# Performance work log

Hardware: AMD Instinct MI355X
Metric: run time of the kernel (lower is better)

Reference implementation:

```python
import math
import jax, jax.numpy as jnp
import numpy as np

CAPACITY_FACTOR = 1.0
MIN_CAPACITY = 4


def setup_inputs() -> dict:
    key = jax.random.key(0)
    k1, k2 = jax.random.split(key)
    x = jax.random.normal(k1, (8192, 1024), dtype=jnp.float32)
    wg = jax.random.normal(k2, (1024, 64), dtype=jnp.float32) * 0.02
    return {"x": x, "wg": wg}


def reference(x, wg):
    # Gate projection: [S, D] @ [D, E] -> [S, E]
    logits = x @ wg
    S, E = logits.shape
    # _capacity: ceil(S / E * capacity_factor * 2) for top-2, floored at min_capacity (static)
    capacity = max(math.ceil((S / E) * (CAPACITY_FACTOR * 2.0)), MIN_CAPACITY)

    gates = jax.nn.softmax(logits, axis=-1)           # [S, E]
    org_gates = gates

    # top-1 expert
    indices1_s = jnp.argmax(gates, axis=1)
    mask1 = jax.nn.one_hot(indices1_s, E, dtype=jnp.int32)
    # top-2 expert (deterministic: no gumbel sampling)
    logits_except1 = jnp.where(mask1.astype(bool), -jnp.inf, logits)
    indices2_s = jnp.argmax(logits_except1, axis=1)
    mask2 = jax.nn.one_hot(indices2_s, E, dtype=jnp.int32)

    # per-expert running positions
    locations1 = jnp.cumsum(mask1, axis=0) - 1        # [S, E]
    locations2 = jnp.cumsum(mask2, axis=0) - 1 + jnp.sum(mask1, axis=0, keepdims=True)

    # load-balancing aux loss
    me = jnp.mean(gates, axis=0)
    ce = jnp.mean(mask1.astype(gates.dtype), axis=0)
    l_aux = jnp.sum(me * ce) * E * E

    exp_counts = jnp.sum(mask1 + mask2, axis=0)

    # drop tokens over capacity
    mask1 = mask1 * (locations1 < capacity).astype(jnp.int32)
    mask2 = mask2 * (locations2 < capacity).astype(jnp.int32)

    locations1_s = jnp.sum(locations1 * mask1, axis=1)  # [S]
    locations2_s = jnp.sum(locations2 * mask2, axis=1)

    mask1_f = mask1.astype(gates.dtype)
    mask2_f = mask2.astype(gates.dtype)
    gates1_s = jnp.sum(gates * mask1_f, axis=1)
    gates2_s = jnp.sum(gates * mask2_f, axis=1)
    denom_s = jnp.clip(gates1_s + gates2_s, jnp.finfo(gates.dtype).eps)
    gates1_s = gates1_s / denom_s
    gates2_s = gates2_s / denom_s

    gates1 = gates1_s[:, None] * mask1_f              # [S, E]
    gates2 = gates2_s[:, None] * mask2_f

    locations1_sc = jax.nn.one_hot(locations1_s, capacity, dtype=gates.dtype)  # [S, C]
    locations2_sc = jax.nn.one_hot(locations2_s, capacity, dtype=gates.dtype)

    combine_weights = (jnp.einsum('se,sc->sec', gates1, locations1_sc)
                       + jnp.einsum('se,sc->sec', gates2, locations2_sc))  # [S, E, C]
    dispatch_mask = combine_weights.astype(bool)
    return l_aux, combine_weights, dispatch_mask, exp_counts, org_gates
```

## Files before the change

kernel.cpp:

```cpp
#include <hip/hip_runtime.h>
#include <math.h>

#define S_TOKENS 8192
#define D_DIM    1024
#define E_EXP    64
#define CAPACITY 256
#define TPB      64
#define NBLK     (S_TOKENS / TPB)
#define NZBLK    4096

typedef float fx4 __attribute__((ext_vector_type(4)));

#define SZ_COMBINE   (134217728LL)
#define OFF_COMBINE  (1LL)
#define OFF_DISPATCH (OFF_COMBINE + SZ_COMBINE)
#define OFF_EXPCNT   (OFF_DISPATCH + SZ_COMBINE)
#define OFF_ORGGATES (OFF_EXPCNT + E_EXP)

#define WS_IDX1 0
#define WS_IDX2 (WS_IDX1 + S_TOKENS)
#define WS_G1   (WS_IDX2 + S_TOKENS)
#define WS_G2   (WS_G1 + S_TOKENS)
#define WS_CNT1 (WS_G2 + S_TOKENS)
#define WS_CNT2 (WS_CNT1 + NBLK * E_EXP)
#define WS_OFF1 (WS_CNT2 + NBLK * E_EXP)
#define WS_OFF2 (WS_OFF1 + NBLK * E_EXP)
#define WS_MEP  (WS_OFF2 + NBLK * E_EXP)

__global__ __launch_bounds__(256) void k1_gemm_gate(
    const float* __restrict__ x, const float* __restrict__ wg,
    float* __restrict__ out, int* __restrict__ wsi, float* __restrict__ wsf) {
  const int bid = blockIdx.x;
  const int tid = threadIdx.x;

  if (bid >= NBLK) {
    fx4 z = (fx4)0.f;
    fx4* p = (fx4*)out;
    const size_t n4 = (size_t)(2 * SZ_COMBINE) / 4;
    const size_t nth = (size_t)NZBLK * 256;
    for (size_t i = (size_t)(bid - NBLK) * 256 + tid; i < n4; i += nth)
      __builtin_nontemporal_store(z, &p[i]);
    if (bid == NBLK && tid == 0) out[2 * SZ_COMBINE] = 0.0f;
    return;
  }

  __shared__ float xs[64][68];
  __shared__ float ovl[64 * 68];
  __shared__ float mM[64], rS[64];
  __shared__ int   li1[64], li2[64];
  __shared__ float mered[16][64];

  float (*wsh)[64] = (float(*)[64])ovl;
  float (*Lg)[68]  = (float(*)[68])ovl;

  const int tx = tid & 15;
  const int ty = tid >> 4;
  const int s0 = bid * TPB;

  float acc[4][4];
#pragma unroll
  for (int i = 0; i < 4; i++)
#pragma unroll
    for (int q = 0; q < 4; q++) acc[i][q] = 0.f;

  for (int k0 = 0; k0 < D_DIM; k0 += 64) {
#pragma unroll
    for (int r = 0; r < 4; r++) {
      int i = tid + 256 * r;
      int t = i >> 4, c = i & 15;
      *(fx4*)&xs[t][4 * c] =
          *(const fx4*)&x[(size_t)(s0 + t) * D_DIM + k0 + 4 * c];
      *(fx4*)&wsh[t][4 * c] =
          *(const fx4*)&wg[(size_t)(k0 + t) * E_EXP + 4 * c];
    }
    __syncthreads();
    for (int kb = 0; kb < 64; kb += 4) {
      fx4 xa[4], wb[4];
#pragma unroll
      for (int i = 0; i < 4; i++) xa[i] = *(fx4*)&xs[ty + 16 * i][kb];
#pragma unroll
      for (int j = 0; j < 4; j++) wb[j] = *(fx4*)&wsh[kb + j][4 * tx];
#pragma unroll
      for (int j = 0; j < 4; j++)
#pragma unroll
        for (int i = 0; i < 4; i++) {
          float xv = xa[i][j];
#pragma unroll
          for (int q = 0; q < 4; q++)
            acc[i][q] = fmaf(xv, wb[j][q], acc[i][q]);
        }
    }
    __syncthreads();
  }

#pragma unroll
  for (int i = 0; i < 4; i++) {
    fx4 v;
#pragma unroll
    for (int q = 0; q < 4; q++) v[q] = acc[i][q];
    *(fx4*)&Lg[ty + 16 * i][4 * tx] = v;
  }
  __syncthreads();

  {
    const int g = tid >> 2;
    const int u = tid & 3;
    float bv = -INFINITY; int bi = 0;
#pragma unroll
    for (int i = 0; i < 16; i++) {
      int ee = u + 4 * i;
      float v = Lg[g][ee];
      if (v > bv) { bv = v; bi = ee; }
    }
#pragma unroll
    for (int d = 1; d < 4; d <<= 1) {
      float ovv = __shfl_xor(bv, d, 4);
      int   oi  = __shfl_xor(bi, d, 4);
      if (ovv > bv || (ovv == bv && oi < bi)) { bv = ovv; bi = oi; }
    }
    const float m1 = bv; const int i1 = bi;

    float se = 0.f;
#pragma unroll
    for (int i = 0; i < 16; i++) se += expf(Lg[g][u + 4 * i] - m1);
#pragma unroll
    for (int d = 1; d < 4; d <<= 1) se += __shfl_xor(se, d, 4);

    float bv2 = -INFINITY; int bi2 = 0;
#pragma unroll
    for (int i = 0; i < 16; i++) {
      int ee = u + 4 * i;
      float v = Lg[g][ee];
      if (ee != i1 && v > bv2) { bv2 = v; bi2 = ee; }
    }
#pragma unroll
    for (int d = 1; d < 4; d <<= 1) {
      float ovv = __shfl_xor(bv2, d, 4);
      int   oi  = __shfl_xor(bi2, d, 4);
      if (ovv > bv2 || (ovv == bv2 && oi < bi2)) { bv2 = ovv; bi2 = oi; }
    }

    if (u == 0) {
      float rs = 1.0f / se;
      mM[g] = m1; rS[g] = rs;
      li1[g] = i1; li2[g] = bi2;
      int s = s0 + g;
      wsi[WS_IDX1 + s] = i1;
      wsi[WS_IDX2 + s] = bi2;
      wsf[WS_G1 + s] = rs;
      wsf[WS_G2 + s] = expf(bv2 - m1) * rs;
    }
  }
  __syncthreads();

  {
    float ms[4] = {0.f, 0.f, 0.f, 0.f};
#pragma unroll
    for (int i = 0; i < 4; i++) {
      int t = ty + 16 * i;
      float m = mM[t], r = rS[t];
      size_t ob = OFF_ORGGATES + (size_t)(s0 + t) * E_EXP + 4 * tx;
#pragma unroll
      for (int q = 0; q < 4; q++) {
        float gate = expf(Lg[t][4 * tx + q] - m) * r;
        out[ob + q] = gate;
        ms[q] += gate;
      }
    }
#pragma unroll
    for (int q = 0; q < 4; q++) mered[ty][4 * tx + q] = ms[q];
  }
  __syncthreads();

  if (tid < 64) {
    float s = 0.f;
#pragma unroll
    for (int yy = 0; yy < 16; yy++) s += mered[yy][tid];
    wsf[WS_MEP + bid * 64 + tid] = s;
    int c1 = 0, c2 = 0;
    for (int t = 0; t < TPB; t++) {
      c1 += (li1[t] == tid);
      c2 += (li2[t] == tid);
    }
    wsi[WS_CNT1 + bid * 64 + tid] = c1;
    wsi[WS_CNT2 + bid * 64 + tid] = c2;
  }
}

__global__ __launch_bounds__(1024) void k2_scan(
    float* __restrict__ out, int* __restrict__ wsi, float* __restrict__ wsf) {
  __shared__ int lc[NBLK * E_EXP];
  __shared__ float mep[16][E_EXP];
  __shared__ int tot1[E_EXP];

  const int tid = threadIdx.x;

  {
    const int e = tid & 63, cg = tid >> 6;
    float s = 0.f;
#pragma unroll
    for (int c = cg * 8; c < cg * 8 + 8; c++) s += wsf[WS_MEP + c * 64 + e];
    mep[cg][e] = s;
  }

  {
    const int4* g = (const int4*)&wsi[WS_CNT1];
    int4* l = (int4*)lc;
#pragma unroll
    for (int i = tid; i < NBLK * E_EXP / 4; i += 1024) l[i] = g[i];
  }
  __syncthreads();

  if (tid < E_EXP) {
    int run = 0;
#pragma unroll 8
    for (int c = 0; c < NBLK; c++) {
      wsi[WS_OFF1 + c * 64 + tid] = run;
      run += lc[c * 64 + tid];
    }
    tot1[tid] = run;
  }
  __syncthreads();

  {
    const int4* g = (const int4*)&wsi[WS_CNT2];
    int4* l = (int4*)lc;
#pragma unroll
    for (int i = tid; i < NBLK * E_EXP / 4; i += 1024) l[i] = g[i];
  }
  __syncthreads();

  if (tid < E_EXP) {
    const int e = tid;
    const int total1 = tot1[e];
    int run = total1;
#pragma unroll 8
    for (int c = 0; c < NBLK; c++) {
      wsi[WS_OFF2 + c * 64 + e] = run;
      run += lc[c * 64 + e];
    }
    const int total2 = run - total1;

    out[OFF_EXPCNT + e] = (float)(total1 + total2);

    float mesum = 0.f;
#pragma unroll
    for (int cg = 0; cg < 16; cg++) mesum += mep[cg][e];
    float me = mesum * (1.0f / 8192.0f);
    float ce = (float)total1 * (1.0f / 8192.0f);
    float prod = me * ce * 4096.0f;
#pragma unroll
    for (int d = 1; d < 64; d <<= 1) prod += __shfl_xor(prod, d, 64);
    if (e == 0) out[0] = prod;
  }
}

__global__ __launch_bounds__(64) void k3_scatter(
    float* __restrict__ out, const int* __restrict__ wsi,
    const float* __restrict__ wsf) {
  __shared__ int li1[TPB], li2[TPB];
  const int bid = blockIdx.x;
  const int t = threadIdx.x;
  const int s0 = bid * TPB;

  li1[t] = wsi[WS_IDX1 + s0 + t];
  li2[t] = wsi[WS_IDX2 + s0 + t];
  __syncthreads();

  const int e1 = li1[t], e2 = li2[t];
  int r1 = 0, r2 = 0;
  for (int j = 0; j < t; j++) {
    r1 += (li1[j] == e1);
    r2 += (li2[j] == e2);
  }
  const int loc1 = wsi[WS_OFF1 + bid * 64 + e1] + r1;
  const int loc2 = wsi[WS_OFF2 + bid * 64 + e2] + r2;
  const int s = s0 + t;

  const float g1r = wsf[WS_G1 + s];
  const float g2r = wsf[WS_G2 + s];
  const bool d1 = (loc1 >= CAPACITY);
  const bool d2 = (loc2 >= CAPACITY);
  const float g1f = d1 ? 0.f : g1r;
  const float g2f = d2 ? 0.f : g2r;
  const float denom = fmaxf(g1f + g2f, 1.1920929e-7f);
  const float w1 = g1f / denom;
  const float w2 = g2f / denom;

  if (!d1) {
    size_t o = OFF_COMBINE + (size_t)s * (E_EXP * CAPACITY) +
               (size_t)e1 * CAPACITY + loc1;
    out[o] = w1;
    out[o + SZ_COMBINE] = (w1 != 0.f) ? 1.f : 0.f;
  }
  if (!d2) {
    size_t o = OFF_COMBINE + (size_t)s * (E_EXP * CAPACITY) +
               (size_t)e2 * CAPACITY + loc2;
    out[o] = w2;
    out[o + SZ_COMBINE] = (w2 != 0.f) ? 1.f : 0.f;
  }
}

extern "C" void kernel_launch(void* const* d_in, const int* in_sizes, int n_in,
                              void* d_out, int out_size, void* d_ws,
                              size_t ws_size, hipStream_t stream) {
  const float* x  = (const float*)d_in[0];
  const float* wg = (const float*)d_in[1];
  float* out = (float*)d_out;
  int*   wsi = (int*)d_ws;
  float* wsf = (float*)d_ws;

  hipLaunchKernelGGL(k1_gemm_gate, dim3(NBLK + NZBLK), dim3(256), 0, stream,
                     x, wg, out, wsi, wsf);
  hipLaunchKernelGGL(k2_scan, dim3(1), dim3(1024), 0, stream, out, wsi, wsf);
  hipLaunchKernelGGL(k3_scatter, dim3(NBLK), dim3(64), 0, stream, out, wsi,
                     wsf);
}
```

Measured before the change: 1.134 ms.

## Fuse scan and scatter kernels into one single-block kernel with LDS offsets

```diff
diff --git a/kernel.cpp b/kernel.cpp
--- a/kernel.cpp
+++ b/kernel.cpp
@@ -23,9 +23,7 @@
 #define WS_G2   (WS_G1 + S_TOKENS)
 #define WS_CNT1 (WS_G2 + S_TOKENS)
 #define WS_CNT2 (WS_CNT1 + NBLK * E_EXP)
-#define WS_OFF1 (WS_CNT2 + NBLK * E_EXP)
-#define WS_OFF2 (WS_OFF1 + NBLK * E_EXP)
-#define WS_MEP  (WS_OFF2 + NBLK * E_EXP)
+#define WS_MEP  (WS_CNT2 + NBLK * E_EXP)
 
 __global__ __launch_bounds__(256) void k1_gemm_gate(
     const float* __restrict__ x, const float* __restrict__ wg,
@@ -187,11 +185,12 @@
   }
 }
 
-__global__ __launch_bounds__(1024) void k2_scan(
-    float* __restrict__ out, int* __restrict__ wsi, float* __restrict__ wsf) {
-  __shared__ int lc[NBLK * E_EXP];
+__global__ __launch_bounds__(1024) void k23_scan_scatter(
+    float* __restrict__ out, const int* __restrict__ wsi,
+    const float* __restrict__ wsf) {
+  __shared__ int off1[NBLK * E_EXP];
+  __shared__ int off2[NBLK * E_EXP];
   __shared__ float mep[16][E_EXP];
-  __shared__ int tot1[E_EXP];
 
   const int tid = threadIdx.x;
 
@@ -204,42 +203,36 @@
   }
 
   {
-    const int4* g = (const int4*)&wsi[WS_CNT1];
-    int4* l = (int4*)lc;
-#pragma unroll
-    for (int i = tid; i < NBLK * E_EXP / 4; i += 1024) l[i] = g[i];
+    const int4* g1 = (const int4*)&wsi[WS_CNT1];
+    const int4* g2 = (const int4*)&wsi[WS_CNT2];
+    int4* l1 = (int4*)off1;
+    int4* l2 = (int4*)off2;
+#pragma unroll
+    for (int i = tid; i < NBLK * E_EXP / 4; i += 1024) {
+      l1[i] = g1[i];
+      l2[i] = g2[i];
+    }
   }
   __syncthreads();
 
   if (tid < E_EXP) {
+    const int e = tid;
     int run = 0;
 #pragma unroll 8
     for (int c = 0; c < NBLK; c++) {
-      wsi[WS_OFF1 + c * 64 + tid] = run;
-      run += lc[c * 64 + tid];
-    }
-    tot1[tid] = run;
-  }
-  __syncthreads();
-
-  {
-    const int4* g = (const int4*)&wsi[WS_CNT2];
-    int4* l = (int4*)lc;
-#pragma unroll
-    for (int i = tid; i < NBLK * E_EXP / 4; i += 1024) l[i] = g[i];
-  }
-  __syncthreads();
-
-  if (tid < E_EXP) {
-    const int e = tid;
-    const int total1 = tot1[e];
-    int run = total1;
+      int v = off1[c * 64 + e];
+      off1[c * 64 + e] = run;
+      run += v;
+    }
+    const int total1 = run;
+    int run2 = total1;
 #pragma unroll 8
     for (int c = 0; c < NBLK; c++) {
-      wsi[WS_OFF2 + c * 64 + e] = run;
-      run += lc[c * 64 + e];
-    }
-    const int total2 = run - total1;
+      int v = off2[c * 64 + e];
+      off2[c * 64 + e] = run2;
+      run2 += v;
+    }
+    const int total2 = run2 - total1;
 
     out[OFF_EXPCNT + e] = (float)(total1 + total2);
 
@@ -253,51 +246,46 @@
     for (int d = 1; d < 64; d <<= 1) prod += __shfl_xor(prod, d, 64);
     if (e == 0) out[0] = prod;
   }
-}
-
-__global__ __launch_bounds__(64) void k3_scatter(
-    float* __restrict__ out, const int* __restrict__ wsi,
-    const float* __restrict__ wsf) {
-  __shared__ int li1[TPB], li2[TPB];
-  const int bid = blockIdx.x;
-  const int t = threadIdx.x;
-  const int s0 = bid * TPB;
-
-  li1[t] = wsi[WS_IDX1 + s0 + t];
-  li2[t] = wsi[WS_IDX2 + s0 + t];
-  __syncthreads();
-
-  const int e1 = li1[t], e2 = li2[t];
-  int r1 = 0, r2 = 0;
-  for (int j = 0; j < t; j++) {
-    r1 += (li1[j] == e1);
-    r2 += (li2[j] == e2);
-  }
-  const int loc1 = wsi[WS_OFF1 + bid * 64 + e1] + r1;
-  const int loc2 = wsi[WS_OFF2 + bid * 64 + e2] + r2;
-  const int s = s0 + t;
-
-  const float g1r = wsf[WS_G1 + s];
-  const float g2r = wsf[WS_G2 + s];
-  const bool d1 = (loc1 >= CAPACITY);
-  const bool d2 = (loc2 >= CAPACITY);
-  const float g1f = d1 ? 0.f : g1r;
-  const float g2f = d2 ? 0.f : g2r;
-  const float denom = fmaxf(g1f + g2f, 1.1920929e-7f);
-  const float w1 = g1f / denom;
-  const float w2 = g2f / denom;
-
-  if (!d1) {
-    size_t o = OFF_COMBINE + (size_t)s * (E_EXP * CAPACITY) +
-               (size_t)e1 * CAPACITY + loc1;
-    out[o] = w1;
-    out[o + SZ_COMBINE] = (w1 != 0.f) ? 1.f : 0.f;
-  }
-  if (!d2) {
-    size_t o = OFF_COMBINE + (size_t)s * (E_EXP * CAPACITY) +
-               (size_t)e2 * CAPACITY + loc2;
-    out[o] = w2;
-    out[o + SZ_COMBINE] = (w2 != 0.f) ? 1.f : 0.f;
+  __syncthreads();
+
+  const int wv = tid >> 6, ln = tid & 63;
+  for (int c = wv; c < NBLK; c += 16) {
+    const int s = c * TPB + ln;
+    const int e1 = wsi[WS_IDX1 + s];
+    const int e2 = wsi[WS_IDX2 + s];
+    int r1 = 0, r2 = 0;
+#pragma unroll 7
+    for (int j = 0; j < TPB - 1; j++) {
+      int o1 = __shfl(e1, j, 64);
+      int o2 = __shfl(e2, j, 64);
+      r1 += (j < ln && o1 == e1);
+      r2 += (j < ln && o2 == e2);
+    }
+    const int loc1 = off1[c * 64 + e1] + r1;
+    const int loc2 = off2[c * 64 + e2] + r2;
+
+    const float g1r = wsf[WS_G1 + s];
+    const float g2r = wsf[WS_G2 + s];
+    const bool d1 = (loc1 >= CAPACITY);
+    const bool d2 = (loc2 >= CAPACITY);
+    const float g1f = d1 ? 0.f : g1r;
+    const float g2f = d2 ? 0.f : g2r;
+    const float denom = fmaxf(g1f + g2f, 1.1920929e-7f);
+    const float w1 = g1f / denom;
+    const float w2 = g2f / denom;
+
+    if (!d1) {
+      size_t o = OFF_COMBINE + (size_t)s * (E_EXP * CAPACITY) +
+                 (size_t)e1 * CAPACITY + loc1;
+      out[o] = w1;
+      out[o + SZ_COMBINE] = (w1 != 0.f) ? 1.f : 0.f;
+    }
+    if (!d2) {
+      size_t o = OFF_COMBINE + (size_t)s * (E_EXP * CAPACITY) +
+                 (size_t)e2 * CAPACITY + loc2;
+      out[o] = w2;
+      out[o + SZ_COMBINE] = (w2 != 0.f) ? 1.f : 0.f;
+    }
   }
 }
 
@@ -312,7 +300,6 @@
 
   hipLaunchKernelGGL(k1_gemm_gate, dim3(NBLK + NZBLK), dim3(256), 0, stream,
                      x, wg, out, wsi, wsf);
-  hipLaunchKernelGGL(k2_scan, dim3(1), dim3(1024), 0, stream, out, wsi, wsf);
-  hipLaunchKernelGGL(k3_scatter, dim3(NBLK), dim3(64), 0, stream, out, wsi,
-                     wsf);
+  hipLaunchKernelGGL(k23_scan_scatter, dim3(1), dim3(1024), 0, stream, out,
+                     wsi, wsf);
 }
```

Measured after the change: 1.174 ms. 3.5% more time.
